# Optimization experiments

Measured on AMD Instinct MI355X. Metric: run time of the kernel, lower is better.

The kernel has to match this reference:

```python
import jax, jax.numpy as jnp
import numpy as np
from itertools import combinations_with_replacement

D = 64
M_MAX = 4


def _build_exponents(D, M):
    # All multiset exponent vectors (degree m monomials) for m = 0..M,
    # matching comb(D+m-1, m) features per order, in combinations_with_replacement order.
    rows, ords = [], []
    for m in range(M + 1):
        for combo in combinations_with_replacement(range(D), m):
            e = np.zeros(D, dtype=np.int32)
            for i in combo:
                e[i] += 1
            rows.append(e)
            ords.append(m)
    return np.stack(rows), np.asarray(ords, dtype=np.int32)


def setup_inputs() -> dict:
    key = jax.random.key(0)
    kx, kw = jax.random.split(key)
    E_np, ord_np = _build_exponents(D, M_MAX)
    F = E_np.shape[0]  # 814385 total monomial features
    x = jax.random.normal(kx, (D,), dtype=jnp.float32)
    w = jax.random.normal(kw, (F,), dtype=jnp.float32)
    # module init: alphas[m] = 1 / 2**m
    alphas = jnp.asarray([1.0 / (2.0 ** m) for m in range(M_MAX + 1)], dtype=jnp.float32)
    return {
        "x": x,
        "w": w,
        "alphas": alphas,
        "E": jnp.asarray(E_np),        # [F, D] int32 exponents (constant)
        "ord_ids": jnp.asarray(ord_np),  # [F] int32 polynomial order per feature
    }


def reference(x, w, alphas, E, ord_ids):
    # phi_f = prod_d x_d ** E[f, d]   -> [F], vectorized monomial basis
    phi = jnp.prod(x[None, :] ** E, axis=1)
    scaled = alphas[ord_ids] * phi  # per-order scaling alphas[m]
    f = jnp.dot(w, scaled)
    return jax.nn.sigmoid(f)
```

## Files before the change

kernel.cpp:

```cpp
#include <hip/hip_runtime.h>
#include <math.h>


#define DVARS 64
#define F_TOTAL 814385u
#define OFF1 1u
#define OFF2 65u
#define OFF3 2145u
#define OFF4 47905u

#define BLOCK 256
#define NBLOCKS ((F_TOTAL + BLOCK - 1) / BLOCK)

__device__ __forceinline__ unsigned ub_search(const unsigned* __restrict__ arr,
                                              unsigned target, unsigned lo) {
    unsigned hi = 63u;
    while (lo < hi) {
        unsigned mid = (lo + hi + 1u) >> 1;
        if (arr[mid] <= target) lo = mid; else hi = mid - 1u;
    }
    return lo;
}

__global__ __launch_bounds__(BLOCK)
void poly_partial_kernel(const float* __restrict__ x,
                         const float* __restrict__ w,
                         const float* __restrict__ alphas,
                         float* __restrict__ partial) {
    __shared__ float xs[DVARS];
    __shared__ float as[5];
    __shared__ unsigned G2[65], G3[65], B4[65];
    __shared__ float wsum[BLOCK / 64];

    const int tid = threadIdx.x;
    if (tid < DVARS) xs[tid] = x[tid];
    if (tid < 5)     as[tid] = alphas[tid];
    if (tid < 65) {
        unsigned a = (unsigned)tid;
        G2[a] = a * 64u - (a * (a - 1u)) / 2u;
        unsigned g3 = 0u, b4 = 0u;
        for (unsigned b = 0u; b < a; ++b) {
            unsigned n = 64u - b;
            g3 += n * (n + 1u) / 2u;
            b4 += n * (n + 1u) * (n + 2u) / 6u;
        }
        G3[a] = g3;
        B4[a] = b4;
    }
    __syncthreads();

    const unsigned f = blockIdx.x * (unsigned)BLOCK + (unsigned)tid;
    float val = 0.0f;
    if (f < F_TOTAL) {
        float phi, alpha;
        if (f == 0u) {
            phi = 1.0f; alpha = as[0];
        } else if (f < OFF2) {
            phi = xs[f - OFF1]; alpha = as[1];
        } else if (f < OFF3) {
            unsigned r = f - OFF2;
            unsigned i = ub_search(G2, r, 0u);
            unsigned j = i + (r - G2[i]);
            phi = xs[i] * xs[j]; alpha = as[2];
        } else if (f < OFF4) {
            unsigned r = f - OFF3;
            unsigned i = ub_search(G3, r, 0u);
            unsigned r2 = r - G3[i];
            unsigned j = ub_search(G2, r2 + G2[i], i);
            unsigned r3 = r2 - (G2[j] - G2[i]);
            unsigned k = j + r3;
            phi = xs[i] * xs[j] * xs[k]; alpha = as[3];
        } else {
            unsigned r = f - OFF4;
            unsigned i = ub_search(B4, r, 0u);
            unsigned r2 = r - B4[i];
            unsigned j = ub_search(G3, r2 + G3[i], i);
            unsigned r3 = r2 - (G3[j] - G3[i]);
            unsigned k = ub_search(G2, r3 + G2[j], j);
            unsigned r4 = r3 - (G2[k] - G2[j]);
            unsigned l = k + r4;
            phi = xs[i] * xs[j] * xs[k] * xs[l]; alpha = as[4];
        }
        val = alpha * phi * w[f];
    }

    #pragma unroll
    for (int off = 32; off > 0; off >>= 1)
        val += __shfl_down(val, off);
    const int wave = tid >> 6;
    if ((tid & 63) == 0) wsum[wave] = val;
    __syncthreads();
    if (tid == 0) {
        float s = 0.0f;
        #pragma unroll
        for (int v = 0; v < BLOCK / 64; ++v) s += wsum[v];
        partial[blockIdx.x] = s;
    }
}

__global__ __launch_bounds__(BLOCK)
void reduce_sigmoid_kernel(const float* __restrict__ partial, int n,
                           float* __restrict__ out) {
    __shared__ float wsum[BLOCK / 64];
    const int tid = threadIdx.x;
    float s = 0.0f;
    for (int idx = tid; idx < n; idx += BLOCK) s += partial[idx];
    #pragma unroll
    for (int off = 32; off > 0; off >>= 1)
        s += __shfl_down(s, off);
    if ((tid & 63) == 0) wsum[tid >> 6] = s;
    __syncthreads();
    if (tid == 0) {
        float fsum = 0.0f;
        #pragma unroll
        for (int v = 0; v < BLOCK / 64; ++v) fsum += wsum[v];
        out[0] = 1.0f / (1.0f + expf(-fsum));
    }
}

extern "C" void kernel_launch(void* const* d_in, const int* in_sizes, int n_in,
                              void* d_out, int out_size, void* d_ws, size_t ws_size,
                              hipStream_t stream) {
    const float* x      = (const float*)d_in[0];
    const float* w      = (const float*)d_in[1];
    const float* alphas = (const float*)d_in[2];
    float* out = (float*)d_out;
    float* partial = (float*)d_ws;

    poly_partial_kernel<<<dim3(NBLOCKS), dim3(BLOCK), 0, stream>>>(x, w, alphas, partial);
    reduce_sigmoid_kernel<<<dim3(1), dim3(BLOCK), 0, stream>>>(partial, (int)NBLOCKS, out);
}
```

Measured before the change: 260.0 us.

## Process eight consecutive order-4 monomials per thread with incremental index stepping

Order-4 features are now handled in groups of eight per thread. Each group runs the three binary searches once for its first index and then steps the (i,j,k,l) multiset index forward in lexicographic order. This amortizes the search cost and cuts the thread and block count, so fewer partials need reducing. Each thread issues eight strided w loads, which hurts coalescing, and the grouping relies on the order-4 count dividing evenly by eight.

```diff
diff --git a/kernel.cpp b/kernel.cpp
--- a/kernel.cpp
+++ b/kernel.cpp
@@ -10,7 +10,10 @@
 #define OFF4 47905u
 
 #define BLOCK 256
-#define NBLOCKS ((F_TOTAL + BLOCK - 1) / BLOCK)
+#define NSINGLE OFF4
+#define NMULTI ((F_TOTAL - OFF4) / 8u)
+#define TOT_THREADS (NSINGLE + NMULTI)
+#define NBLOCKS ((TOT_THREADS + BLOCK - 1) / BLOCK)
 
 __device__ __forceinline__ unsigned ub_search(const unsigned* __restrict__ arr,
                                               unsigned target, unsigned lo) {
@@ -49,9 +52,10 @@
     }
     __syncthreads();
 
-    const unsigned f = blockIdx.x * (unsigned)BLOCK + (unsigned)tid;
+    const unsigned gt = blockIdx.x * (unsigned)BLOCK + (unsigned)tid;
     float val = 0.0f;
-    if (f < F_TOTAL) {
+    if (gt < NSINGLE) {
+        const unsigned f = gt;
         float phi, alpha;
         if (f == 0u) {
             phi = 1.0f; alpha = as[0];
@@ -62,7 +66,7 @@
             unsigned i = ub_search(G2, r, 0u);
             unsigned j = i + (r - G2[i]);
             phi = xs[i] * xs[j]; alpha = as[2];
-        } else if (f < OFF4) {
+        } else {
             unsigned r = f - OFF3;
             unsigned i = ub_search(G3, r, 0u);
             unsigned r2 = r - G3[i];
@@ -70,31 +74,45 @@
             unsigned r3 = r2 - (G2[j] - G2[i]);
             unsigned k = j + r3;
             phi = xs[i] * xs[j] * xs[k]; alpha = as[3];
-        } else {
-            unsigned r = f - OFF4;
-            unsigned i = ub_search(B4, r, 0u);
-            unsigned r2 = r - B4[i];
-            unsigned j = ub_search(G3, r2 + G3[i], i);
-            unsigned r3 = r2 - (G3[j] - G3[i]);
-            unsigned k = ub_search(G2, r3 + G2[j], j);
-            unsigned r4 = r3 - (G2[k] - G2[j]);
-            unsigned l = k + r4;
-            phi = xs[i] * xs[j] * xs[k] * xs[l]; alpha = as[4];
         }
         val = alpha * phi * w[f];
+    } else if (gt < TOT_THREADS) {
+        const unsigned t  = gt - NSINGLE;
+        const unsigned f0 = OFF4 + 8u * t;
+        unsigned r = 8u * t;
+        unsigned i = ub_search(B4, r, 0u);
+        unsigned r2 = r - B4[i];
+        unsigned j = ub_search(G3, r2 + G3[i], i);
+        unsigned r3 = r2 - (G3[j] - G3[i]);
+        unsigned k = ub_search(G2, r3 + G2[j], j);
+        unsigned l = k + (r3 - (G2[k] - G2[j]));
+
+        float wv[8];
+        #pragma unroll
+        for (int q = 0; q < 8; ++q) wv[q] = w[f0 + (unsigned)q];
+
+        float s = 0.0f;
+        #pragma unroll
+        for (int q = 0; q < 8; ++q) {
+            s += wv[q] * (xs[i] * xs[j] * xs[k] * xs[l]);
+            if (l < 63u)      { ++l; }
+            else if (k < 63u) { ++k; l = k; }
+            else if (j < 63u) { ++j; k = j; l = j; }
+            else              { ++i; j = i; k = i; l = i; }
+        }
+        val = as[4] * s;
     }
 
     #pragma unroll
     for (int off = 32; off > 0; off >>= 1)
         val += __shfl_down(val, off);
-    const int wave = tid >> 6;
-    if ((tid & 63) == 0) wsum[wave] = val;
+    if ((tid & 63) == 0) wsum[tid >> 6] = val;
     __syncthreads();
     if (tid == 0) {
-        float s = 0.0f;
+        float sb = 0.0f;
         #pragma unroll
-        for (int v = 0; v < BLOCK / 64; ++v) s += wsum[v];
-        partial[blockIdx.x] = s;
+        for (int v = 0; v < BLOCK / 64; ++v) sb += wsum[v];
+        partial[blockIdx.x] = sb;
     }
 }
 
```

New measurement: 247.9 us. 4.7% less time.
